# Optimization experiments

Hardware: AMD Instinct MI355X
Metric: run time of the kernel (lower is better)

## Reference

```python
import jax, jax.numpy as jnp
import numpy as np

B, IN_UNITS, C, U, K = 32, 16, 8192, 32, 16
NUM_ITERS = 3


def setup_inputs() -> dict:
    key = jax.random.key(0)
    k1, k2 = jax.random.split(key)
    x = jax.random.normal(k1, (B, IN_UNITS, C), dtype=jnp.float32)
    # W corresponds to the torch parameter of shape (1, C, U, K, IN_UNITS), leading 1 dropped
    W = jax.random.normal(k2, (C, U, K, IN_UNITS), dtype=jnp.float32)
    return {"x": x, "W": W}


def reference(x, W):
    batch = x.shape[0]
    # u_hat[b,c,u,k] = sum_i W[c,u,k,i] * x[b,i,c]   (torch: W @ x after transpose/stack)
    u_hat = jnp.einsum('cuki,bic->bcuk', W, x)
    b_ij = jnp.zeros((C, U), dtype=x.dtype)
    v = None
    for _ in range(NUM_ITERS):
        c_ij = jax.nn.softmax(b_ij, axis=0)            # softmax over in_channels (dim=1 in torch)
        s = jnp.einsum('cu,bcuk->buk', c_ij, u_hat)    # weighted sum over channels
        # squash: note the original sums over dim=2 of (B,1,U,K,1) == the num_units axis
        mag_sq = jnp.sum(s ** 2, axis=1, keepdims=True)  # (B,1,K)
        mag = jnp.sqrt(mag_sq)
        v = mag_sq / (1.0 + mag_sq) * (s / mag)          # (B,U,K)
        # agreement: mean over batch of <u_hat, v>
        a = jnp.einsum('bcuk,buk->cu', u_hat, v) / batch
        b_ij = b_ij + a
    return v[..., None]  # matches torch output (B, num_units, unit_size, 1)
```

## Files before the change

### kernel.cpp

```cpp
#include <hip/hip_runtime.h>

#define CC   8192
#define UU   32
#define KK   16
#define BB   32
#define INU  16
#define UK   512
#define CPB  32
#define NBLK 256

__global__ __launch_bounds__(512, 2) void fused_pass(
    const float* __restrict__ x, const float* __restrict__ W,
    const float* __restrict__ v_in, float* __restrict__ b_io,
    float* __restrict__ S, float* __restrict__ Z)
{
    __shared__ float xs[16 * 516];

    const int t   = threadIdx.x;
    const int bid = blockIdx.x;
    const int c0  = bid * CPB;
    const int u   = t >> 4;
    const int k   = t & 15;

    float v[BB], Sl[BB], uh[BB];
#pragma unroll
    for (int b = 0; b < BB; ++b) { v[b] = v_in[b * UK + t]; Sl[b] = 0.f; }
    float zloc = 0.f;

    float4 w0, w1, w2, w3;
    {
        const float4* p = (const float4*)(W + ((size_t)c0 * UK + t) * INU);
        w0 = p[0]; w1 = p[1]; w2 = p[2]; w3 = p[3];
    }

    for (int cc = 0; cc < CPB; ++cc) {
        if ((cc & 15) == 0) {
            __syncthreads();
            const int cbase = c0 + (cc & ~15);
            for (int j = 0; j < 16; ++j) {
                int idx = j * 512 + t;
                int ccl = idx & 15;
                int bi  = idx >> 4;
                xs[ccl * 516 + bi] = x[bi * CC + cbase + ccl];
            }
            __syncthreads();
        }

        float4 n0, n1, n2, n3;
        const bool have_next = (cc + 1 < CPB);
        if (have_next) {
            const float4* p = (const float4*)(W + ((size_t)(c0 + cc + 1) * UK + t) * INU);
            n0 = p[0]; n1 = p[1]; n2 = p[2]; n3 = p[3];
        }

        const float* xrow = &xs[(cc & 15) * 516];
        float ap = 0.f;
#pragma unroll
        for (int b = 0; b < BB; ++b) {
            const float4* xr = (const float4*)(xrow + b * INU);
            float4 x0 = xr[0], x1 = xr[1], x2 = xr[2], x3 = xr[3];
            float h;
            h = w0.x * x0.x;
            h = fmaf(w0.y, x0.y, h); h = fmaf(w0.z, x0.z, h); h = fmaf(w0.w, x0.w, h);
            h = fmaf(w1.x, x1.x, h); h = fmaf(w1.y, x1.y, h);
            h = fmaf(w1.z, x1.z, h); h = fmaf(w1.w, x1.w, h);
            h = fmaf(w2.x, x2.x, h); h = fmaf(w2.y, x2.y, h);
            h = fmaf(w2.z, x2.z, h); h = fmaf(w2.w, x2.w, h);
            h = fmaf(w3.x, x3.x, h); h = fmaf(w3.y, x3.y, h);
            h = fmaf(w3.z, x3.z, h); h = fmaf(w3.w, x3.w, h);
            uh[b] = h;
            ap = fmaf(h, v[b], ap);
        }

        ap += __shfl_xor(ap, 8);
        ap += __shfl_xor(ap, 4);
        ap += __shfl_xor(ap, 2);
        ap += __shfl_xor(ap, 1);

        const int c = c0 + cc;
        float bnew = b_io[c * UU + u] + ap * (1.0f / (float)BB);
        float e = __expf(bnew);
        zloc += e;
        if (k == 0) b_io[c * UU + u] = bnew;

#pragma unroll
        for (int b = 0; b < BB; ++b) Sl[b] = fmaf(e, uh[b], Sl[b]);

        if (have_next) { w0 = n0; w1 = n1; w2 = n2; w3 = n3; }
    }

#pragma unroll
    for (int b = 0; b < BB; ++b) atomicAdd(S + b * UK + t, Sl[b]);
    if (k == 0) atomicAdd(Z + u, zloc);
}

__global__ void squash_k(const float* __restrict__ S, const float* __restrict__ Z,
                         float* __restrict__ vout)
{
    __shared__ float z_sh[UU];
    __shared__ float s2_sh[UK];
    __shared__ float mag_sh[KK];

    const int b = blockIdx.x;
    const int t = threadIdx.x;

    if (t < UU) z_sh[t] = Z[t];
    float ssum = S[b * UK + t];
    __syncthreads();

    float s = ssum / z_sh[t >> 4];
    s2_sh[t] = s * s;
    __syncthreads();

    if (t < KK) {
        float m = 0.f;
        for (int uu = 0; uu < UU; ++uu) m += s2_sh[uu * KK + t];
        mag_sh[t] = m;
    }
    __syncthreads();

    float msq = mag_sh[t & 15];
    float out = (msq / (1.0f + msq)) * s / sqrtf(msq);
    vout[b * UK + t] = out;
}

extern "C" void kernel_launch(void* const* d_in, const int* in_sizes, int n_in,
                              void* d_out, int out_size, void* d_ws, size_t ws_size,
                              hipStream_t stream)
{
    const float* x = (const float*)d_in[0];
    const float* W = (const float*)d_in[1];
    float* out = (float*)d_out;

    char* ws = (char*)d_ws;
    float* S   = (float*)(ws);
    float* Z   = (float*)(ws + 65536);
    float* vb  = (float*)(ws + 65536 + 256);
    float* bio = (float*)(ws + 65536 + 256 + 65536);

    hipMemsetAsync(vb,  0, BB * UK * 4, stream);
    hipMemsetAsync(bio, 0, CC * UU * 4, stream);

    for (int pass = 0; pass < 3; ++pass) {
        hipMemsetAsync(S, 0, BB * UK * 4, stream);
        hipMemsetAsync(Z, 0, UU * 4, stream);
        fused_pass<<<NBLK, 512, 0, stream>>>(x, W, vb, bio, S, Z);
        float* vo = (pass == 2) ? out : vb;
        squash_k<<<BB, UK, 0, stream>>>(S, Z, vo);
    }
}
```

Before: 705.3 us.

## Remap threads to batch-group x four-units tiles with DPP reductions and merged memsets

```diff
diff --git a/kernel.cpp b/kernel.cpp
--- a/kernel.cpp
+++ b/kernel.cpp
@@ -2,96 +2,141 @@
 
 #define CC   8192
 #define UU   32
-#define KK   16
 #define BB   32
 #define INU  16
 #define UK   512
 #define CPB  32
 #define NBLK 256
+#define XS_STRIDE 528
+
+template <int CTRL>
+__device__ __forceinline__ float dpp_add(float x) {
+  int p = __builtin_amdgcn_update_dpp(0, __float_as_int(x), CTRL, 0xF, 0xF, true);
+  return x + __int_as_float(p);
+}
 
 __global__ __launch_bounds__(512, 2) void fused_pass(
     const float* __restrict__ x, const float* __restrict__ W,
     const float* __restrict__ v_in, float* __restrict__ b_io,
-    float* __restrict__ S, float* __restrict__ Z)
+    float* __restrict__ S, float* __restrict__ Z, const int iter0)
 {
-    __shared__ float xs[16 * 516];
+    __shared__ float xs[16 * XS_STRIDE];
 
-    const int t   = threadIdx.x;
-    const int bid = blockIdx.x;
-    const int c0  = bid * CPB;
-    const int u   = t >> 4;
-    const int k   = t & 15;
+    const int t  = threadIdx.x;
+    const int w  = t >> 6;
+    const int l  = t & 63;
+    const int k  = l & 15;
+    const int bg = l >> 4;
+    const int u0 = w * 4;
+    const int c0 = blockIdx.x * CPB;
 
-    float v[BB], Sl[BB], uh[BB];
+    float v[4][8], Sl[4][8];
 #pragma unroll
-    for (int b = 0; b < BB; ++b) { v[b] = v_in[b * UK + t]; Sl[b] = 0.f; }
-    float zloc = 0.f;
+    for (int j = 0; j < 4; ++j)
+#pragma unroll
+      for (int bb = 0; bb < 8; ++bb) Sl[j][bb] = 0.f;
 
-    float4 w0, w1, w2, w3;
-    {
-        const float4* p = (const float4*)(W + ((size_t)c0 * UK + t) * INU);
-        w0 = p[0]; w1 = p[1]; w2 = p[2]; w3 = p[3];
+    if (iter0) {
+#pragma unroll
+      for (int j = 0; j < 4; ++j)
+#pragma unroll
+        for (int bb = 0; bb < 8; ++bb) v[j][bb] = 0.f;
+    } else {
+#pragma unroll
+      for (int j = 0; j < 4; ++j)
+#pragma unroll
+        for (int bb = 0; bb < 8; ++bb)
+          v[j][bb] = v_in[(bg * 8 + bb) * UK + (u0 + j) * 16 + k];
     }
+    float zloc[4] = {0.f, 0.f, 0.f, 0.f};
 
     for (int cc = 0; cc < CPB; ++cc) {
         if ((cc & 15) == 0) {
             __syncthreads();
             const int cbase = c0 + (cc & ~15);
-            for (int j = 0; j < 16; ++j) {
-                int idx = j * 512 + t;
+#pragma unroll
+            for (int jj = 0; jj < 16; ++jj) {
+                int idx = jj * 512 + t;
                 int ccl = idx & 15;
                 int bi  = idx >> 4;
-                xs[ccl * 516 + bi] = x[bi * CC + cbase + ccl];
+                int b   = bi >> 4, i = bi & 15;
+                xs[ccl * XS_STRIDE + (b & 7) * 64 + (b >> 3) * 16 + i] = x[bi * CC + cbase + ccl];
             }
             __syncthreads();
         }
 
-        float4 n0, n1, n2, n3;
-        const bool have_next = (cc + 1 < CPB);
-        if (have_next) {
-            const float4* p = (const float4*)(W + ((size_t)(c0 + cc + 1) * UK + t) * INU);
-            n0 = p[0]; n1 = p[1]; n2 = p[2]; n3 = p[3];
+        const int c = c0 + cc;
+
+        float bold[4] = {0.f, 0.f, 0.f, 0.f};
+        if (!iter0) {
+#pragma unroll
+            for (int j = 0; j < 4; ++j) bold[j] = b_io[(size_t)c * UU + u0 + j];
         }
 
-        const float* xrow = &xs[(cc & 15) * 516];
-        float ap = 0.f;
+        float4 wq[4][4];
+        {
+            const float4* wp = (const float4*)(W + ((size_t)c * UK + (size_t)u0 * 16 + k) * INU);
 #pragma unroll
-        for (int b = 0; b < BB; ++b) {
-            const float4* xr = (const float4*)(xrow + b * INU);
-            float4 x0 = xr[0], x1 = xr[1], x2 = xr[2], x3 = xr[3];
-            float h;
-            h = w0.x * x0.x;
-            h = fmaf(w0.y, x0.y, h); h = fmaf(w0.z, x0.z, h); h = fmaf(w0.w, x0.w, h);
-            h = fmaf(w1.x, x1.x, h); h = fmaf(w1.y, x1.y, h);
-            h = fmaf(w1.z, x1.z, h); h = fmaf(w1.w, x1.w, h);
-            h = fmaf(w2.x, x2.x, h); h = fmaf(w2.y, x2.y, h);
-            h = fmaf(w2.z, x2.z, h); h = fmaf(w2.w, x2.w, h);
-            h = fmaf(w3.x, x3.x, h); h = fmaf(w3.y, x3.y, h);
-            h = fmaf(w3.z, x3.z, h); h = fmaf(w3.w, x3.w, h);
-            uh[b] = h;
-            ap = fmaf(h, v[b], ap);
+            for (int j = 0; j < 4; ++j)
+#pragma unroll
+                for (int q = 0; q < 4; ++q) wq[j][q] = wp[j * 64 + q];
         }
 
-        ap += __shfl_xor(ap, 8);
-        ap += __shfl_xor(ap, 4);
-        ap += __shfl_xor(ap, 2);
-        ap += __shfl_xor(ap, 1);
-
-        const int c = c0 + cc;
-        float bnew = b_io[c * UU + u] + ap * (1.0f / (float)BB);
-        float e = __expf(bnew);
-        zloc += e;
-        if (k == 0) b_io[c * UU + u] = bnew;
+        float uh[4][8];
+        float ap[4] = {0.f, 0.f, 0.f, 0.f};
+        const float* xrow = &xs[(cc & 15) * XS_STRIDE + bg * 16];
+#pragma unroll
+        for (int bb = 0; bb < 8; ++bb) {
+            const float4* xr = (const float4*)(xrow + bb * 64);
+            float4 x0 = xr[0], x1 = xr[1], x2 = xr[2], x3 = xr[3];
+#pragma unroll
+            for (int j = 0; j < 4; ++j) {
+                float h;
+                h = wq[j][0].x * x0.x;
+                h = fmaf(wq[j][0].y, x0.y, h); h = fmaf(wq[j][0].z, x0.z, h); h = fmaf(wq[j][0].w, x0.w, h);
+                h = fmaf(wq[j][1].x, x1.x, h); h = fmaf(wq[j][1].y, x1.y, h);
+                h = fmaf(wq[j][1].z, x1.z, h); h = fmaf(wq[j][1].w, x1.w, h);
+                h = fmaf(wq[j][2].x, x2.x, h); h = fmaf(wq[j][2].y, x2.y, h);
+                h = fmaf(wq[j][2].z, x2.z, h); h = fmaf(wq[j][2].w, x2.w, h);
+                h = fmaf(wq[j][3].x, x3.x, h); h = fmaf(wq[j][3].y, x3.y, h);
+                h = fmaf(wq[j][3].z, x3.z, h); h = fmaf(wq[j][3].w, x3.w, h);
+                uh[j][bb] = h;
+                ap[j] = fmaf(h, v[j][bb], ap[j]);
+            }
+        }
 
 #pragma unroll
-        for (int b = 0; b < BB; ++b) Sl[b] = fmaf(e, uh[b], Sl[b]);
+        for (int j = 0; j < 4; ++j) {
+            float a = ap[j];
+            a = dpp_add<0xB1>(a);
+            a = dpp_add<0x4E>(a);
+            a = dpp_add<0x141>(a);
+            a = dpp_add<0x140>(a);
+            a += __shfl_xor(a, 16);
+            a += __shfl_xor(a, 32);
+            ap[j] = a;
+        }
 
-        if (have_next) { w0 = n0; w1 = n1; w2 = n2; w3 = n3; }
+#pragma unroll
+        for (int j = 0; j < 4; ++j) {
+            float bnew = bold[j] + ap[j] * (1.0f / 32.0f);
+            float e = __expf(bnew);
+            zloc[j] += e;
+            if (l == 0) b_io[(size_t)c * UU + u0 + j] = bnew;
+#pragma unroll
+            for (int bb = 0; bb < 8; ++bb) Sl[j][bb] = fmaf(e, uh[j][bb], Sl[j][bb]);
+        }
     }
 
 #pragma unroll
-    for (int b = 0; b < BB; ++b) atomicAdd(S + b * UK + t, Sl[b]);
-    if (k == 0) atomicAdd(Z + u, zloc);
+    for (int j = 0; j < 4; ++j)
+#pragma unroll
+        for (int bb = 0; bb < 8; ++bb)
+            atomicAdd(S + (bg * 8 + bb) * UK + (u0 + j) * 16 + k, Sl[j][bb]);
+    if (l == 0) {
+#pragma unroll
+        for (int j = 0; j < 4; ++j) atomicAdd(Z + u0 + j, zloc[j]);
+    }
 }
 
 __global__ void squash_k(const float* __restrict__ S, const float* __restrict__ Z,
@@ -99,7 +144,7 @@
 {
     __shared__ float z_sh[UU];
     __shared__ float s2_sh[UK];
-    __shared__ float mag_sh[KK];
+    __shared__ float mag_sh[16];
 
     const int b = blockIdx.x;
     const int t = threadIdx.x;
@@ -112,9 +157,9 @@
     s2_sh[t] = s * s;
     __syncthreads();
 
-    if (t < KK) {
+    if (t < 16) {
         float m = 0.f;
-        for (int uu = 0; uu < UU; ++uu) m += s2_sh[uu * KK + t];
+        for (int uu = 0; uu < UU; ++uu) m += s2_sh[uu * 16 + t];
         mag_sh[t] = m;
     }
     __syncthreads();
@@ -133,19 +178,16 @@
     float* out = (float*)d_out;
 
     char* ws = (char*)d_ws;
-    float* S   = (float*)(ws);
-    float* Z   = (float*)(ws + 65536);
-    float* vb  = (float*)(ws + 65536 + 256);
-    float* bio = (float*)(ws + 65536 + 256 + 65536);
+    const size_t SLOT = 65536 + 256;
+    float* vb  = (float*)(ws + 3 * SLOT);
+    float* bio = (float*)(ws + 3 * SLOT + 65536);
 
-    hipMemsetAsync(vb,  0, BB * UK * 4, stream);
-    hipMemsetAsync(bio, 0, CC * UU * 4, stream);
+    hipMemsetAsync(ws, 0, 3 * SLOT, stream);
 
     for (int pass = 0; pass < 3; ++pass) {
-        hipMemsetAsync(S, 0, BB * UK * 4, stream);
-        hipMemsetAsync(Z, 0, UU * 4, stream);
-        fused_pass<<<NBLK, 512, 0, stream>>>(x, W, vb, bio, S, Z);
-        float* vo = (pass == 2) ? out : vb;
-        squash_k<<<BB, UK, 0, stream>>>(S, Z, vo);
+        float* S = (float*)(ws + pass * SLOT);
+        float* Z = (float*)(ws + pass * SLOT + 65536);
+        fused_pass<<<NBLK, 512, 0, stream>>>(x, W, vb, bio, S, Z, pass == 0 ? 1 : 0);
+        squash_k<<<BB, 512, 0, stream>>>(S, Z, (pass == 2) ? out : vb);
     }
 }
```

Result: slower. 770.2 us (+9.2%).
